# Performance work log

Measured on AMD Instinct MI355X. Metric: run time of the kernel, lower is better.

The kernel has to match this reference:

```python
import jax, jax.numpy as jnp
import numpy as np
import math

B, S, D, H = 2, 2048, 1024, 16
DH = D // H  # head_size = 64


def setup_inputs() -> dict:
    key = jax.random.key(0)
    ks = jax.random.split(key, 11)
    s = 0.02
    return {
        "queries": jax.random.normal(ks[0], (B, S, D), jnp.float32),
        "keys": jax.random.normal(ks[1], (B, S, D), jnp.float32),
        "values": jax.random.normal(ks[2], (B, S, D), jnp.float32),
        # nn.Linear weights: y = x @ W.T + b, W has shape (out, in)
        "W_Q": jax.random.normal(ks[3], (D, D), jnp.float32) * s,
        "b_Q": jax.random.normal(ks[4], (D,), jnp.float32) * s,
        "W_K": jax.random.normal(ks[5], (D, D), jnp.float32) * s,
        "b_K": jax.random.normal(ks[6], (D,), jnp.float32) * s,
        "W_V": jax.random.normal(ks[7], (D, D), jnp.float32) * s,
        "b_V": jax.random.normal(ks[8], (D,), jnp.float32) * s,
        "W_O": jax.random.normal(ks[9], (D, D), jnp.float32) * s,
        "b_O": jax.random.normal(ks[10], (D,), jnp.float32) * s,
    }


def _split_heads(x):
    # (B, S, H*DH) -> (B, H, S, DH); torch.chunk+stack == reshape+transpose
    b, s, _ = x.shape
    return x.reshape(b, s, H, DH).transpose(0, 2, 1, 3)


def reference(queries, keys, values, W_Q, b_Q, W_K, b_K, W_V, b_V, W_O, b_O):
    q = _split_heads(queries @ W_Q.T + b_Q)  # (B,H,S,DH)
    k = _split_heads(keys @ W_K.T + b_K)
    v = _split_heads(values @ W_V.T + b_V)

    scale = 1.0 / math.sqrt(DH)
    scores = jnp.einsum("bhqd,bhkd->bhqk", q, k) * scale  # (B,H,S,S)
    causal = jnp.tril(jnp.ones((S, S), dtype=bool))  # allow j <= i (causal)
    scores = jnp.where(causal, scores, -jnp.inf)
    weights = jax.nn.softmax(scores, axis=-1)

    attended = jnp.einsum("bhqk,bhkd->bhqd", weights, v)  # (B,H,S,DH)
    merged = attended.transpose(0, 2, 1, 3).reshape(B, S, D)  # merge_heads
    return merged @ W_O.T + b_O
```

## Files before the change

kernel.cpp:

```cpp
#include <hip/hip_runtime.h>


typedef __bf16 bf16x8 __attribute__((ext_vector_type(8)));
typedef __bf16 bf16x4 __attribute__((ext_vector_type(4)));
typedef float  f32x4  __attribute__((ext_vector_type(4)));
typedef int    i32x2  __attribute__((ext_vector_type(2)));
typedef int    i32x4  __attribute__((ext_vector_type(4)));

#define B_  2
#define S_  2048
#define D_  1024
#define H_  16
#define DH_ 64

#define NEG_ 1.0e30f
#define M2_  5.77078016f
#define QSCALE_ 0.18033688f

#if __has_builtin(__builtin_amdgcn_exp2f)
#define EXP2(x) __builtin_amdgcn_exp2f(x)
#else
#define EXP2(x) __builtin_exp2f(x)
#endif

__device__ __forceinline__ void load_lds16(const __bf16* g, __bf16* lds_base) {
    __builtin_amdgcn_global_load_lds(
        (const __attribute__((address_space(1))) void*)g,
        (__attribute__((address_space(3))) void*)lds_base,
        16, 0, 0);
}

__device__ __forceinline__ int pack_bf16(float lo, float hi) {
    union { int u; __bf16 h[2]; } r;
    r.h[0] = (__bf16)lo; r.h[1] = (__bf16)hi;
    return r.u;
}

__device__ __forceinline__ void p32swap(int& a, int& b, int lane) {
#if __has_builtin(__builtin_amdgcn_permlane32_swap)
    i32x2 r = __builtin_amdgcn_permlane32_swap(a, b, false, false);
    a = r[0]; b = r[1];
#else
    const int addr = ((lane ^ 32) & 63) << 2;
    int ax = __builtin_amdgcn_ds_bpermute(addr, a);
    int bx = __builtin_amdgcn_ds_bpermute(addr, b);
    int na = (lane < 32) ? a : bx;
    int nb = (lane < 32) ? ax : b;
    a = na; b = nb;
#endif
}
__device__ __forceinline__ void p16swap(int& a, int& b, int lane) {
#if __has_builtin(__builtin_amdgcn_permlane16_swap)
    i32x2 r = __builtin_amdgcn_permlane16_swap(a, b, false, false);
    a = r[0]; b = r[1];
#else
    int as = __builtin_amdgcn_ds_swizzle(a, 0x401F);
    int bs = __builtin_amdgcn_ds_swizzle(b, 0x401F);
    const bool odd = (lane >> 4) & 1;
    int na = odd ? bs : a;
    int nb = odd ? b : as;
    a = na; b = nb;
#endif
}

__device__ __forceinline__ bf16x8 cvt8(const float* __restrict__ p) {
    const float4 a = *(const float4*)p;
    const float4 b = *(const float4*)(p + 4);
    bf16x8 r;
    r[0] = (__bf16)a.x; r[1] = (__bf16)a.y; r[2] = (__bf16)a.z; r[3] = (__bf16)a.w;
    r[4] = (__bf16)b.x; r[5] = (__bf16)b.y; r[6] = (__bf16)b.z; r[7] = (__bf16)b.w;
    return r;
}

__global__ void cvt_kernel(const float* __restrict__ q, const float* __restrict__ k,
                           const float* __restrict__ v,
                           const float* __restrict__ wq, const float* __restrict__ wk,
                           const float* __restrict__ wv, const float* __restrict__ wo,
                           __bf16* __restrict__ qb, __bf16* __restrict__ kb,
                           __bf16* __restrict__ vb,
                           __bf16* __restrict__ wqb, __bf16* __restrict__ wkb,
                           __bf16* __restrict__ wvb, __bf16* __restrict__ wob) {
    const int z = blockIdx.z;
    const float* src; __bf16* dst; size_t n;
    switch (z) {
        case 0: src = q;  dst = qb;  n = (size_t)B_ * S_ * D_; break;
        case 1: src = k;  dst = kb;  n = (size_t)B_ * S_ * D_; break;
        case 2: src = v;  dst = vb;  n = (size_t)B_ * S_ * D_; break;
        case 3: src = wq; dst = wqb; n = (size_t)D_ * D_; break;
        case 4: src = wk; dst = wkb; n = (size_t)D_ * D_; break;
        case 5: src = wv; dst = wvb; n = (size_t)D_ * D_; break;
        default: src = wo; dst = wob; n = (size_t)D_ * D_; break;
    }
    const size_t i = ((size_t)blockIdx.x * 256 + threadIdx.x) * 8;
    if (i >= n) return;
    *(bf16x8*)(dst + i) = cvt8(src + i);
}

__device__ __forceinline__ void gemm128_bf(const __bf16* __restrict__ X,
                                           const __bf16* __restrict__ W,
                                           int m0, int n0, int K,
                                           __bf16* As, __bf16* Bs,
                                           f32x4 acc[4][4]) {
    const int tid  = threadIdx.x;
    const int wave = tid >> 6, lane = tid & 63;
    const int row  = lane & 15, quad = lane >> 4;
    const int wm   = wave >> 1, wn = wave & 1;
    const int arow = lane >> 2;
    const int acol = (lane & 3) * 8;

    const f32x4 fzero = {0.f, 0.f, 0.f, 0.f};
#pragma unroll
    for (int mt = 0; mt < 4; ++mt)
#pragma unroll
        for (int nt = 0; nt < 4; ++nt) acc[mt][nt] = fzero;

    auto stage = [&](int buf, int k0) {
#pragma unroll
        for (int c = 0; c < 2; ++c) {
            const int j = wave * 2 + c;
            load_lds16(X + (size_t)(m0 + j * 16 + arow) * K + k0 + acol,
                       As + buf * 4096 + j * 512);
            load_lds16(W + (size_t)(n0 + j * 16 + arow) * K + k0 + acol,
                       Bs + buf * 4096 + j * 512);
        }
    };

    stage(0, 0);
    if (K > 32) stage(1, 32);
    int cur = 0;
    for (int k0 = 0; k0 < K; k0 += 32) {
        if (k0 + 32 < K) asm volatile("s_waitcnt vmcnt(4)" ::: "memory");
        else             asm volatile("s_waitcnt vmcnt(0)" ::: "memory");
        __builtin_amdgcn_s_barrier();
        __builtin_amdgcn_sched_barrier(0);
        if (k0 + 64 < K) {
            int nxt2 = cur + 2; if (nxt2 >= 3) nxt2 -= 3;
            stage(nxt2, k0 + 64);
        }
        const __bf16* Ab = As + cur * 4096;
        const __bf16* Bb = Bs + cur * 4096;
        bf16x8 af[4], bfv[4];
#pragma unroll
        for (int t = 0; t < 4; ++t) {
            af[t]  = *(const bf16x8*)(Ab + (wm * 64 + t * 16 + row) * 32 + quad * 8);
            bfv[t] = *(const bf16x8*)(Bb + (wn * 64 + t * 16 + row) * 32 + quad * 8);
        }
        __builtin_amdgcn_s_setprio(1);
#pragma unroll
        for (int mt = 0; mt < 4; ++mt)
#pragma unroll
            for (int nt = 0; nt < 4; ++nt)
                acc[mt][nt] = __builtin_amdgcn_mfma_f32_16x16x32_bf16(
                    af[mt], bfv[nt], acc[mt][nt], 0, 0, 0);
        __builtin_amdgcn_s_setprio(0);
        if (++cur >= 3) cur = 0;
    }
    __builtin_amdgcn_s_barrier();
}

__global__ void qkv_kernel(const __bf16* __restrict__ qb, const __bf16* __restrict__ kb,
                           const __bf16* __restrict__ vb,
                           const __bf16* __restrict__ wqb, const __bf16* __restrict__ wkb,
                           const __bf16* __restrict__ wvb,
                           const float* __restrict__ bq, const float* __restrict__ bk,
                           const float* __restrict__ bv,
                           __bf16* __restrict__ q_ws, __bf16* __restrict__ k_ws,
                           __bf16* __restrict__ v_ws) {
    __shared__ __align__(16) __bf16 SMEM[24576];
    __bf16* As = SMEM;
    __bf16* Bs = SMEM + 12288;

    const int mode = blockIdx.z;
    const __bf16* X    = mode == 0 ? qb : mode == 1 ? kb : vb;
    const __bf16* W    = mode == 0 ? wqb : mode == 1 ? wkb : wvb;
    const float*  bias = mode == 0 ? bq : mode == 1 ? bk : bv;
    const int m0 = blockIdx.y * 128, n0 = blockIdx.x * 128;

    f32x4 acc[4][4];
    gemm128_bf(X, W, m0, n0, D_, As, Bs, acc);

    const int tid = threadIdx.x;
    const int wave = tid >> 6, lane = tid & 63;
    const int row = lane & 15, quad = lane >> 4;
    const int wm = wave >> 1, wn = wave & 1;

    if (mode == 2) {
        __bf16* T = SMEM;
#pragma unroll
        for (int nt = 0; nt < 4; ++nt) {
            const int nloc = wn * 64 + nt * 16 + row;
            const float bf = bias[n0 + nloc];
#pragma unroll
            for (int mt = 0; mt < 4; ++mt)
#pragma unroll
                for (int r2 = 0; r2 < 4; ++r2) {
                    const int mloc = wm * 64 + mt * 16 + quad * 4 + r2;
                    T[nloc * 128 + ((((mloc >> 3) ^ (nloc & 15)) << 3) | (mloc & 7))] =
                        (__bf16)(acc[mt][nt][r2] + bf);
                }
        }
        __syncthreads();
#pragma unroll
        for (int p = 0; p < 8; ++p) {
            const int nloc = p * 16 + (tid >> 4);
            const int k = tid & 15;
            bf16x8 vv = *(const bf16x8*)(T + nloc * 128 + ((k ^ (nloc & 15)) << 3));
            const int n = n0 + nloc;
            const int h = n >> 6, dh = n & 63;
            const int m = m0 + k * 8;
            const int bb = m >> 11, s = m & (S_ - 1);
            *(bf16x8*)(v_ws + (((size_t)bb * H_ + h) * DH_ + dh) * S_ + s) = vv;
        }
        return;
    }

#pragma unroll
    for (int nt = 0; nt < 4; ++nt) {
        const int n  = n0 + wn * 64 + nt * 16 + row;
        const float bf = bias[n];
        const int h = n >> 6, dh = n & 63;
#pragma unroll
        for (int mt = 0; mt < 4; ++mt) {
#pragma unroll
            for (int r2 = 0; r2 < 4; ++r2) {
                const int m = m0 + wm * 64 + mt * 16 + quad * 4 + r2;
                const int bb = m >> 11, s = m & (S_ - 1);
                const float val = acc[mt][nt][r2] + bf;
                if (mode == 0)
                    q_ws[(((size_t)bb * H_ + h) * S_ + s) * DH_ + dh] = (__bf16)(val * QSCALE_);
                else
                    k_ws[(((size_t)bb * H_ + h) * S_ + s) * DH_ + dh] = (__bf16)val;
            }
        }
    }
}

__global__ __launch_bounds__(256, 4)
void attn_kernel(const __bf16* __restrict__ q_ws, const __bf16* __restrict__ k_ws,
                 const __bf16* __restrict__ v_ws, __bf16* __restrict__ att) {
    __shared__ __align__(16) __bf16 Ks[2 * 64 * 64];
    __shared__ __align__(16) __bf16 Vs[2 * 64 * 64];

    const int id = blockIdx.x;
    const int bh = (id & 7) * 4 + ((id >> 3) & 3);
    const int u = id >> 5, ua = u >> 3, uj = u & 7;
    const int qt = ua * 8 + ((ua & 1) ? (7 - uj) : uj);
    const int tid = threadIdx.x, wave = tid >> 6, lane = tid & 63;
    const int row = lane & 15, quad = lane >> 4;

    const __bf16* Qg = q_ws + ((size_t)bh * S_ + qt * 64 + wave * 16) * DH_;
    const __bf16* Kg = k_ws + (size_t)bh * S_ * DH_;
    const __bf16* Vg = v_ws + (size_t)bh * DH_ * S_;

    bf16x8 qf[2];
#pragma unroll
    for (int ks = 0; ks < 2; ++ks)
        qf[ks] = *(const bf16x8*)(Qg + row * DH_ + ks * 32 + quad * 8);

    bf16x8 onesf;
#pragma unroll
    for (int i = 0; i < 8; ++i) onesf[i] = (__bf16)1.0f;

    const f32x4 fzero = {0.f, 0.f, 0.f, 0.f};
    const f32x4 m2init = {-M2_, -M2_, -M2_, -M2_};
    f32x4 oacc[4];
    f32x4 lacc = fzero;
#pragma unroll
    for (int dt = 0; dt < 4; ++dt) oacc[dt] = fzero;

    const int srow = lane >> 3;
    const int scol = ((lane & 7) ^ srow) * 8;
    const int nkv = qt + 1;

    auto stage = [&](int buf, int kv) {
        __bf16* Kd = Ks + buf * 4096;
        __bf16* Vd = Vs + buf * 4096;
#pragma unroll
        for (int c = 0; c < 2; ++c) {
            const int ck = wave * 2 + c;
            load_lds16(Kg + (size_t)(kv * 64 + ck * 8 + srow) * DH_ + scol, Kd + ck * 512);
            load_lds16(Vg + (size_t)(ck * 8 + srow) * S_ + kv * 64 + scol, Vd + ck * 512);
        }
    };

    stage(0, 0);
    int cur = 0;
    for (int kv = 0; kv < nkv; ++kv) {
        __syncthreads();
        if (kv + 1 < nkv) stage(cur ^ 1, kv + 1);
        const bool diag = (kv == nkv - 1);
        const __bf16* Kb = Ks + cur * 4096;
        const __bf16* Vb = Vs + cur * 4096;
        const int swz = (row & 7) << 3;

#pragma unroll
        for (int kc = 0; kc < 2; ++kc) {
            f32x4 s[2];
            s[0] = m2init; s[1] = m2init;
            __builtin_amdgcn_s_setprio(1);
#pragma unroll
            for (int jn = 0; jn < 2; ++jn) {
                const int nt = kc * 2 + jn;
                const int kb = (nt * 16 + row) * 64 + quad * 8;
                bf16x8 kf0 = *(const bf16x8*)(Kb + (kb ^ swz));
                bf16x8 kf1 = *(const bf16x8*)(Kb + ((kb + 32) ^ swz));
                s[jn] = __builtin_amdgcn_mfma_f32_16x16x32_bf16(kf0, qf[0], s[jn], 0, 0, 0);
                s[jn] = __builtin_amdgcn_mfma_f32_16x16x32_bf16(kf1, qf[1], s[jn], 0, 0, 0);
            }
            __builtin_amdgcn_s_setprio(0);

            if (diag) {
                const int rloc = wave * 16 + row;
#pragma unroll
                for (int jn = 0; jn < 2; ++jn)
#pragma unroll
                    for (int r = 0; r < 4; ++r) {
                        const int cloc = kc * 32 + jn * 16 + quad * 4 + r;
                        if (cloc > rloc) s[jn][r] = -NEG_;
                    }
            }

            float p0[4], p1[4];
#pragma unroll
            for (int r = 0; r < 4; ++r) {
                p0[r] = EXP2(s[0][r]);
                p1[r] = EXP2(s[1][r]);
            }
            int a0 = pack_bf16(p0[0], p0[1]), a1 = pack_bf16(p0[2], p0[3]);
            int b0 = pack_bf16(p1[0], p1[1]), b1 = pack_bf16(p1[2], p1[3]);
            p32swap(a0, b0, lane); p16swap(a0, b0, lane);
            p32swap(a1, b1, lane); p16swap(a1, b1, lane);
            union { i32x4 i; bf16x8 v; } pu;
            pu.i = (i32x4){a0, a1, b0, b1};
            const bf16x8 pf = pu.v;

            __builtin_amdgcn_s_setprio(1);
#pragma unroll
            for (int dt = 0; dt < 4; ++dt) {
                const int vb = (dt * 16 + row) * 64 + kc * 32 + quad * 8;
                bf16x8 vf = *(const bf16x8*)(Vb + (vb ^ swz));
                oacc[dt] = __builtin_amdgcn_mfma_f32_16x16x32_bf16(vf, pf, oacc[dt], 0, 0, 0);
            }
            lacc = __builtin_amdgcn_mfma_f32_16x16x32_bf16(onesf, pf, lacc, 0, 0, 0);
            __builtin_amdgcn_s_setprio(0);
        }
        cur ^= 1;
    }

    const int b = bh >> 4, h = bh & 15;
    const float inv = 1.f / lacc[0];
    const int srow2 = qt * 64 + wave * 16 + row;
    __bf16* obase = att + ((size_t)b * S_ + srow2) * D_ + h * DH_;
#pragma unroll
    for (int dt = 0; dt < 4; ++dt) {
        bf16x4 o;
#pragma unroll
        for (int r = 0; r < 4; ++r) o[r] = (__bf16)(oacc[dt][r] * inv);
        *(bf16x4*)(obase + dt * 16 + quad * 4) = o;
    }
}

__global__ void oproj_kernel(const __bf16* __restrict__ attn, const __bf16* __restrict__ wob,
                             const float* __restrict__ bo, float* __restrict__ out) {
    __shared__ __align__(16) __bf16 SMEM[24576];
    __bf16* As = SMEM;
    __bf16* Bs = SMEM + 12288;
    const int m0 = blockIdx.y * 128, n0 = blockIdx.x * 128;

    f32x4 acc[4][4];
    gemm128_bf(attn, wob, m0, n0, D_, As, Bs, acc);

    const int tid = threadIdx.x;
    const int wave = tid >> 6, lane = tid & 63;
    const int row = lane & 15, quad = lane >> 4;
    const int wm = wave >> 1, wn = wave & 1;

#pragma unroll
    for (int nt = 0; nt < 4; ++nt) {
        const int n = n0 + wn * 64 + nt * 16 + row;
        const float bf = bo[n];
#pragma unroll
        for (int mt = 0; mt < 4; ++mt) {
#pragma unroll
            for (int r = 0; r < 4; ++r) {
                const int m = m0 + wm * 64 + mt * 16 + quad * 4 + r;
                out[(size_t)m * D_ + n] = acc[mt][nt][r] + bf;
            }
        }
    }
}

extern "C" void kernel_launch(void* const* d_in, const int* in_sizes, int n_in,
                              void* d_out, int out_size, void* d_ws, size_t ws_size,
                              hipStream_t stream) {
    const float* q_in = (const float*)d_in[0];
    const float* k_in = (const float*)d_in[1];
    const float* v_in = (const float*)d_in[2];
    const float* wq   = (const float*)d_in[3];
    const float* bq   = (const float*)d_in[4];
    const float* wk   = (const float*)d_in[5];
    const float* bk   = (const float*)d_in[6];
    const float* wv   = (const float*)d_in[7];
    const float* bv   = (const float*)d_in[8];
    const float* wo   = (const float*)d_in[9];
    const float* bo   = (const float*)d_in[10];

    char* ws = (char*)d_ws;
    const size_t MB = 1024 * 1024;
    __bf16* qb   = (__bf16*)(ws);
    __bf16* kb   = (__bf16*)(ws + 8 * MB);
    __bf16* vb   = (__bf16*)(ws + 16 * MB);
    __bf16* wqb  = (__bf16*)(ws + 24 * MB);
    __bf16* wkb  = (__bf16*)(ws + 26 * MB);
    __bf16* wvb  = (__bf16*)(ws + 28 * MB);
    __bf16* wob  = (__bf16*)(ws + 30 * MB);
    __bf16* q_ws = (__bf16*)(ws + 32 * MB);
    __bf16* k_ws = (__bf16*)(ws + 40 * MB);
    __bf16* v_ws = (__bf16*)(ws + 48 * MB);
    __bf16* attb = qb;
    float*  out  = (float*)d_out;

    cvt_kernel<<<dim3(2048, 1, 7), 256, 0, stream>>>(
        q_in, k_in, v_in, wq, wk, wv, wo, qb, kb, vb, wqb, wkb, wvb, wob);
    qkv_kernel<<<dim3(D_ / 128, (B_ * S_) / 128, 3), 256, 0, stream>>>(
        qb, kb, vb, wqb, wkb, wvb, bq, bk, bv, q_ws, k_ws, v_ws);
    attn_kernel<<<dim3(32 * 32), 256, 0, stream>>>(q_ws, k_ws, v_ws, attb);
    oproj_kernel<<<dim3(D_ / 128, (B_ * S_) / 128), 256, 0, stream>>>(attb, wob, bo, out);
}
```

Measured before the change: 207.3 us.

## Triple-buffer K in LDS and load V directly from global into registers

The attention kernel now keeps only K in shared memory, using a three-slot ring with two tiles in flight and explicit vmcnt waits plus a raw s_barrier instead of __syncthreads. V tiles are no longer staged through LDS; each wave loads its V fragments straight from global memory into registers at the top of each kv iteration. The aim is to cut LDS traffic and barrier overhead and to overlap K prefetch more deeply. In exchange, every wave issues redundant global V loads, register pressure rises, and the vmcnt counting is fragile because the V register loads also count toward vmcnt.

```diff
diff --git a/kernel.cpp b/kernel.cpp
--- a/kernel.cpp
+++ b/kernel.cpp
@@ -238,8 +238,7 @@
 __global__ __launch_bounds__(256, 4)
 void attn_kernel(const __bf16* __restrict__ q_ws, const __bf16* __restrict__ k_ws,
                  const __bf16* __restrict__ v_ws, __bf16* __restrict__ att) {
-    __shared__ __align__(16) __bf16 Ks[2 * 64 * 64];
-    __shared__ __align__(16) __bf16 Vs[2 * 64 * 64];
+    __shared__ __align__(16) __bf16 Ks[3 * 64 * 64];
 
     const int id = blockIdx.x;
     const int bh = (id & 7) * 4 + ((id >> 3) & 3);
@@ -272,25 +271,39 @@
     const int scol = ((lane & 7) ^ srow) * 8;
     const int nkv = qt + 1;
 
-    auto stage = [&](int buf, int kv) {
-        __bf16* Kd = Ks + buf * 4096;
-        __bf16* Vd = Vs + buf * 4096;
+    auto stageK = [&](int buf, int kv) {
 #pragma unroll
         for (int c = 0; c < 2; ++c) {
             const int ck = wave * 2 + c;
-            load_lds16(Kg + (size_t)(kv * 64 + ck * 8 + srow) * DH_ + scol, Kd + ck * 512);
-            load_lds16(Vg + (size_t)(ck * 8 + srow) * S_ + kv * 64 + scol, Vd + ck * 512);
+            load_lds16(Kg + (size_t)(kv * 64 + ck * 8 + srow) * DH_ + scol,
+                       Ks + buf * 4096 + ck * 512);
         }
     };
 
-    stage(0, 0);
+    stageK(0, 0);
+    if (nkv > 1) stageK(1, 1);
     int cur = 0;
     for (int kv = 0; kv < nkv; ++kv) {
-        __syncthreads();
-        if (kv + 1 < nkv) stage(cur ^ 1, kv + 1);
+        if (kv + 1 < nkv) asm volatile("s_waitcnt vmcnt(2)" ::: "memory");
+        else              asm volatile("s_waitcnt vmcnt(0)" ::: "memory");
+        __builtin_amdgcn_s_barrier();
+        __builtin_amdgcn_sched_barrier(0);
+
+        bf16x8 vreg[2][4];
+#pragma unroll
+        for (int kc = 0; kc < 2; ++kc)
+#pragma unroll
+            for (int dt = 0; dt < 4; ++dt)
+                vreg[kc][dt] = *(const bf16x8*)(
+                    Vg + (size_t)(dt * 16 + row) * S_ + kv * 64 + kc * 32 + quad * 8);
+
+        if (kv + 2 < nkv) {
+            int nxt2 = cur + 2; if (nxt2 >= 3) nxt2 -= 3;
+            stageK(nxt2, kv + 2);
+        }
+
         const bool diag = (kv == nkv - 1);
         const __bf16* Kb = Ks + cur * 4096;
-        const __bf16* Vb = Vs + cur * 4096;
         const int swz = (row & 7) << 3;
 
 #pragma unroll
@@ -336,15 +349,13 @@
 
             __builtin_amdgcn_s_setprio(1);
 #pragma unroll
-            for (int dt = 0; dt < 4; ++dt) {
-                const int vb = (dt * 16 + row) * 64 + kc * 32 + quad * 8;
-                bf16x8 vf = *(const bf16x8*)(Vb + (vb ^ swz));
-                oacc[dt] = __builtin_amdgcn_mfma_f32_16x16x32_bf16(vf, pf, oacc[dt], 0, 0, 0);
-            }
+            for (int dt = 0; dt < 4; ++dt)
+                oacc[dt] = __builtin_amdgcn_mfma_f32_16x16x32_bf16(
+                    vreg[kc][dt], pf, oacc[dt], 0, 0, 0);
             lacc = __builtin_amdgcn_mfma_f32_16x16x32_bf16(onesf, pf, lacc, 0, 0, 0);
             __builtin_amdgcn_s_setprio(0);
         }
-        cur ^= 1;
+        if (++cur >= 3) cur = 0;
     }
 
     const int b = bh >> 4, h = bh & 15;
```

After: 249.2 us. +20.2%, slower.
